# Optimization experiments

Measured on AMD Instinct MI355X. Metric: run time of the kernel, lower is better.

## Reference

```python
import jax, jax.numpy as jnp
import numpy as np

B, T, HID, MC, L, NCLS = 256, 128, 64, 30, 2, 100


def _flow(x, t, fW0, fb0, fW1, fb1, fW2, fb2, ftw):
    # Continuous affine coupling flow (stribor). x: [..., S, HID], t: [..., S, 1]
    hid = x.shape[-1]
    base = (jnp.arange(hid) < hid // 2).astype(x.dtype)  # ordered_0 mask
    for l in range(fW0.shape[0]):
        m = base if l % 2 == 0 else 1.0 - base
        z = x * m
        a = jnp.tanh(jnp.concatenate([z, t], -1) @ fW0[l] + fb0[l])
        a = jnp.tanh(a @ fW1[l] + fb1[l])
        ss = a @ fW2[l] + fb2[l]                      # [..., 2*hid]
        scale, shift = jnp.split(ss, 2, -1)
        t_scale, t_shift = jnp.split(jnp.tanh(t * ftw[l]), 2, -1)  # TimeTanh
        x = z + (1.0 - m) * (x * jnp.exp(scale * t_scale) + shift * t_shift)
    return x


def setup_inputs() -> dict:
    key = jax.random.key(0)
    ks = jax.random.split(key, 12)
    n = lambda k, s, sc=0.1: jax.random.normal(k, s, dtype=jnp.float32) * sc
    return {
        "times": jax.random.uniform(ks[0], (B, T, 1), dtype=jnp.float32),
        "marks": jax.random.randint(ks[1], (B, T, 1), 0, NCLS),
        "mask": jnp.ones((B, T, 1), jnp.float32),
        "u": jax.random.uniform(ks[2], (T, MC, 1), dtype=jnp.float32),
        "emb": n(ks[3], (NCLS, HID), 1.0),
        "fW0": n(ks[4], (L, HID + 1, HID)),
        "fb0": jnp.zeros((L, HID), jnp.float32),
        "fW1": n(ks[5], (L, HID, HID)),
        "fb1": jnp.zeros((L, HID), jnp.float32),
        "fW2": n(ks[6], (L, HID, 2 * HID)),
        "fb2": jnp.zeros((L, 2 * HID), jnp.float32),
        "ftw": n(ks[7], (L, 2 * HID), 1.0),
        "Wi": n(ks[8], (HID, 1)),
        "bi": jnp.zeros((1,), jnp.float32),
        "W_ih": n(ks[9], (4 * HID, 1 + HID)),
        "W_hh": n(ks[10], (4 * HID, HID)),
        "b_ih": jnp.zeros((4 * HID,), jnp.float32),
        "b_hh": jnp.zeros((4 * HID,), jnp.float32),
    }


def reference(times, marks, mask, u, emb, fW0, fb0, fW1, fb1, fW2, fb2, ftw,
              Wi, bi, W_ih, W_hh, b_ih, b_hh):
    Bn, Tn, _ = times.shape
    hid = emb.shape[1]
    mc = u.shape[1]
    marks_e = emb[marks[..., 0]]      # [B,T,hid]
    m1 = marks_e[:, 1]                # source uses marks[:, 1] every step (faithful)
    inten = lambda x: jax.nn.softplus(x @ Wi + bi)

    def step(carry, xs):
        h, c = carry                  # h,c: [B,hid]
        t, u_i = xs                   # t: [B,1], u_i: [mc,1]
        t3 = t[:, None, :]            # [B,1,1]
        ts = u_i[None] * t3           # [B,mc,1] MC time samples in [0,t)
        xb = jnp.broadcast_to(h[:, None, :], (Bn, mc, hid))
        path = _flow(xb, ts, fW0, fb0, fW1, fb1, fW2, fb2, ftw)   # [B,mc,hid]
        integral = inten(path).mean(1, keepdims=True) * t3        # [B,1,1]
        h2 = _flow(h[:, None, :], t3, fW0, fb0, fW1, fb1, fW2, fb2, ftw)  # [B,1,hid]
        lam = inten(h2)                                           # [B,1,1]
        gates = jnp.concatenate([t, m1], -1) @ W_ih.T + b_ih + h2[:, 0] @ W_hh.T + b_hh
        ig, fg, gg, og = jnp.split(gates, 4, -1)
        c_n = jax.nn.sigmoid(fg) * c + jax.nn.sigmoid(ig) * jnp.tanh(gg)
        h_n = jax.nn.sigmoid(og) * jnp.tanh(c_n)
        nll = -jnp.log(lam[:, 0]) + integral[:, 0]                # [B,1]
        return (h_n, c_n), (h2[:, 0], nll)

    h0 = jnp.zeros((Bn, hid), times.dtype)
    (_, _), (hidden, nll) = jax.lax.scan(step, (h0, h0), (jnp.swapaxes(times, 0, 1), u))
    hidden = jnp.swapaxes(hidden, 0, 1)                           # [B,T,hid]
    loss = (jnp.swapaxes(nll, 0, 1)[:, :, :] * mask[..., 0][..., None]).sum() / mask.sum()
    return loss, hidden
```

## Files before the change

### kernel.cpp

```cpp
#include <hip/hip_runtime.h>
#include <hip/hip_bf16.h>
#include <math.h>

#define Bn   256
#define Tn   128
#define HID  64
#define MCn  30

typedef __attribute__((ext_vector_type(8))) short bf16x8;
typedef __attribute__((ext_vector_type(4))) float f32x4;

__device__ __forceinline__ float rcp_(float x) { return __builtin_amdgcn_rcpf(x); }
__device__ __forceinline__ float tanhf_(float x) {
    float e = __expf(-2.0f * x);
    return __builtin_fmaf(2.0f, rcp_(1.0f + e), -1.0f);
}
__device__ __forceinline__ float sigmoidf_(float x) {
    return rcp_(1.0f + __expf(-x));
}
__device__ __forceinline__ float softplusf_(float z) {
    float e = __expf(-fabsf(z));
    return fmaxf(z, 0.0f) + __logf(1.0f + e);
}
__device__ __forceinline__ unsigned short f2b(float f) {
    union { float f; unsigned u; } v; v.f = f;
    unsigned r = v.u + 0x7FFF + ((v.u >> 16) & 1);
    return (unsigned short)(r >> 16);
}
__device__ __forceinline__ unsigned pk2(float a, float b) {
    union { __hip_bfloat162 h2; unsigned u; } cv;
    cv.h2 = __float22bfloat162_rn(make_float2(a, b));
    return cv.u;
}

extern "C" __global__ __launch_bounds__(256)
void prep_kernel(const int* __restrict__ marks, const float* __restrict__ mask,
                 const float* __restrict__ emb, const float* __restrict__ fW0,
                 const float* __restrict__ fW1, const float* __restrict__ fW2,
                 const float* __restrict__ fb0, const float* __restrict__ fb1,
                 const float* __restrict__ fb2, const float* __restrict__ ftw,
                 const float* __restrict__ Wi, const float* __restrict__ W_ih,
                 const float* __restrict__ W_hh,
                 const float* __restrict__ b_ih, const float* __restrict__ b_hh,
                 float* __restrict__ gc, float* __restrict__ invd,
                 float* __restrict__ parv, unsigned short* __restrict__ parwb,
                 float* __restrict__ seqw1T, float* __restrict__ seqw2T,
                 float* __restrict__ whh260)
{
    __shared__ float red[4];
    const int blk = blockIdx.x, tid = threadIdx.x;
    if (blk < Bn) {
        const int mark = marks[blk * Tn + 1];
        const float* er = emb + mark * HID;
        const float* wr = W_ih + tid * 65 + 1;
        float acc = b_ih[tid] + b_hh[tid];
        #pragma unroll
        for (int k = 0; k < HID; k++) acc += er[k] * wr[k];
        gc[blk * 256 + tid] = acc;
    } else if (blk == Bn) {
        float s = 0.f;
        for (int i = tid; i < Bn * Tn; i += 256) s += mask[i];
        #pragma unroll
        for (int off = 32; off >= 1; off >>= 1) s += __shfl_xor(s, off, 64);
        if ((tid & 63) == 0) red[tid >> 6] = s;
        __syncthreads();
        if (tid == 0) invd[0] = 1.0f / (red[0] + red[1] + red[2] + red[3]);
    } else if (blk == Bn + 1) {
        if (tid < 128) {
            int l = tid >> 6, m = tid & 63;
            parv[tid]       = fb0[tid];
            parv[128 + tid] = fW0[(l * 65 + 64) * 64 + m];
            parv[256 + tid] = fb1[tid];
            int act = 32 * (1 - l);
            parv[384 + tid] = fb2[l * 128 + act + (m & 31) + 64 * (m >> 5)];
        }
        if (tid < 64) {
            int l = tid >> 5, i2 = tid & 31, act = 32 * (1 - l);
            parv[512 + tid] = ftw[l * 128 + act + i2];
            parv[576 + tid] = ftw[l * 128 + 64 + act + i2];
            parv[640 + tid] = Wi[tid];
            parv[704 + tid] = 0.f;
        }
    } else if (blk == Bn + 2) {
        for (int i = tid; i < 5120; i += 256) {
            int k = i % 40, m = (i / 40) & 63, l = i / 2560;
            float v = (k < 32) ? fW0[(l * 65 + 32 * l + k) * 64 + m] : 0.f;
            parwb[i] = f2b(v);
        }
    } else if (blk == Bn + 3) {
        for (int i = tid; i < 9216; i += 256) {
            int k = i % 72, m = (i / 72) & 63, l = i / 4608;
            float v = (k < 64) ? fW1[(l * 64 + k) * 64 + m] : 0.f;
            parwb[5120 + i] = f2b(v);
        }
    } else if (blk == Bn + 4) {
        for (int i = tid; i < 9216; i += 256) {
            int k = i % 72, m = (i / 72) & 63, l = i / 4608;
            int act = 32 * (1 - l);
            float v = (k < 64) ? fW2[(l * 64 + k) * 128 + act + (m & 31) + 64 * (m >> 5)] : 0.f;
            parwb[14336 + i] = f2b(v);
        }
    } else if (blk == Bn + 5) {
        for (int i = tid; i < 8704; i += 256) {
            int k = i % 68, j = (i / 68) & 63, l = i / 4352;
            seqw1T[i] = (k < 64) ? fW1[(l * 64 + k) * 64 + j] : 0.f;
        }
    } else if (blk == Bn + 6) {
        for (int i = tid; i < 8704; i += 256) {
            int k = i % 68, j = (i / 68) & 63, l = i / 4352;
            int act = 32 * (1 - l);
            seqw2T[i] = (k < 64) ?
                fW2[(l * 64 + k) * 128 + act + (j & 31) + 64 * (j >> 5)] : 0.f;
        }
    } else {
        for (int i = tid; i < 16640; i += 256) {
            int j = i / 260, rem = i % 260, k = rem >> 2, r = rem & 3;
            whh260[i] = (k < 64) ? W_hh[(r * 64 + j) * 64 + k] : 0.f;
        }
    }
}

extern "C" __global__ __launch_bounds__(64, 1)
void seq_kernel(const float* __restrict__ times, const float* __restrict__ mask,
                const float* __restrict__ fW0, const float* __restrict__ fb0,
                const float* __restrict__ fb1, const float* __restrict__ fb2,
                const float* __restrict__ ftw, const float* __restrict__ Wi,
                const float* __restrict__ bi, const float* __restrict__ W_ih,
                const float* __restrict__ gc, const float* __restrict__ seqw1T,
                const float* __restrict__ invd,
                float* __restrict__ h_carry, float* __restrict__ out)
{
    const int j = threadIdx.x;
    const int b = blockIdx.x;

    extern __shared__ float smem[];
    float* w1l  = smem;
    float* w2l  = smem + 8704;
    float* whhl = smem + 17408;
    float* tl   = smem + 34048;
    float* ml   = smem + 34176;
    float* xl   = smem + 34304;
    float* al   = smem + 34368;
    float* ssl  = smem + 34432;

    {
        const float4* s = (const float4*)seqw1T;
        float4* d = (float4*)smem;
        for (int i = j; i < 8512; i += 64) d[i] = s[i];
    }
    tl[j] = times[b * Tn + j];       tl[j + 64] = times[b * Tn + 64 + j];
    ml[j] = mask[b * Tn + j];        ml[j + 64] = mask[b * Tn + 64 + j];

    float w0c[2][32], w0tc[2], b0c[2], b1c[2], b2c[2], ftsc[2], ftsh[2];
    #pragma unroll
    for (int l = 0; l < 2; l++) {
        #pragma unroll
        for (int kk = 0; kk < 32; kk++)
            w0c[l][kk] = fW0[(l * 65 + 32 * l + kk) * 64 + j];
        w0tc[l] = fW0[(l * 65 + 64) * 64 + j];
        b0c[l]  = fb0[l * 64 + j];
        b1c[l]  = fb1[l * 64 + j];
        const int act = 32 * (1 - l);
        b2c[l]  = fb2[l * 128 + act + (j & 31) + 64 * (j >> 5)];
        ftsc[l] = ftw[l * 128 + j];
        ftsh[l] = ftw[l * 128 + 64 + j];
    }
    const float wij = Wi[j];
    const float bi0 = bi[0];
    float wih0[4], gcr[4];
    #pragma unroll
    for (int r = 0; r < 4; r++) {
        wih0[r] = W_ih[(r * 64 + j) * 65];
        gcr[r]  = gc[b * 256 + r * 64 + j];
    }
    const float idn = invd[0];

    float h = 0.f, c = 0.f, nllacc = 0.f;
    for (int t = 0; t < Tn; t++) {
        const float tb = tl[t];
        float tscv[2], tshv[2];
        #pragma unroll
        for (int l = 0; l < 2; l++) {
            tscv[l] = tanhf_(tb * ftsc[l]);
            tshv[l] = tanhf_(tb * ftsh[l]);
        }
        h_carry[(b * Tn + t) * 64 + j] = h;
        float x = h;
        xl[j] = x;
        #pragma unroll
        for (int l = 0; l < 2; l++) {
            const int kb  = 32 * l;
            const int act = 32 * (1 - l);
            float p0 = b0c[l] + tb * w0tc[l], p1 = 0.f, p2 = 0.f, p3 = 0.f;
            {
                const float4* xv4 = (const float4*)(xl + kb);
                #pragma unroll
                for (int k4 = 0; k4 < 8; k4++) {
                    float4 xv = xv4[k4];
                    p0 += xv.x * w0c[l][4 * k4 + 0];
                    p1 += xv.y * w0c[l][4 * k4 + 1];
                    p2 += xv.z * w0c[l][4 * k4 + 2];
                    p3 += xv.w * w0c[l][4 * k4 + 3];
                }
            }
            al[j] = tanhf_((p0 + p1) + (p2 + p3));
            p0 = b1c[l]; p1 = p2 = p3 = 0.f;
            {
                const float4* av4 = (const float4*)al;
                const float*  wp  = w1l + (l * 64 + j) * 68;
                #pragma unroll
                for (int k4 = 0; k4 < 16; k4++) {
                    float4 av = av4[k4];
                    float4 wv = *(const float4*)(wp + 4 * k4);
                    p0 += av.x * wv.x;
                    p1 += av.y * wv.y;
                    p2 += av.z * wv.z;
                    p3 += av.w * wv.w;
                }
            }
            al[j] = tanhf_((p0 + p1) + (p2 + p3));
            p0 = b2c[l]; p1 = p2 = p3 = 0.f;
            {
                const float4* av4 = (const float4*)al;
                const float*  wp  = w2l + (l * 64 + j) * 68;
                #pragma unroll
                for (int k4 = 0; k4 < 16; k4++) {
                    float4 av = av4[k4];
                    float4 wv = *(const float4*)(wp + 4 * k4);
                    p0 += av.x * wv.x;
                    p1 += av.y * wv.y;
                    p2 += av.z * wv.z;
                    p3 += av.w * wv.w;
                }
            }
            ssl[j] = (p0 + p1) + (p2 + p3);
            const int idx = (j - act) & 31;
            const float scl = ssl[idx];
            const float shf = ssl[idx + 32];
            const float xa  = x * __expf(scl * tscv[l]) + shf * tshv[l];
            const bool active = (l == 0) ? (j >= 32) : (j < 32);
            x = active ? xa : x;
            xl[j] = x;
        }
        out[1 + (b * Tn + t) * 64 + j] = x;
        float v = x * wij;
        #pragma unroll
        for (int off = 32; off >= 1; off >>= 1) v += __shfl_xor(v, off, 64);
        nllacc += -__logf(softplusf_(v + bi0)) * ml[t];
        float g0 = gcr[0] + tb * wih0[0];
        float g1 = gcr[1] + tb * wih0[1];
        float g2 = gcr[2] + tb * wih0[2];
        float g3 = gcr[3] + tb * wih0[3];
        {
            const float*  wr_base = whhl + j * 260;
            const float4* hv4 = (const float4*)xl;
            #pragma unroll
            for (int k4 = 0; k4 < 16; k4++) {
                float4 hv = hv4[k4];
                const float* wr = wr_base + 16 * k4;
                float4 wa = *(const float4*)(wr);
                float4 wb = *(const float4*)(wr + 4);
                float4 wc = *(const float4*)(wr + 8);
                float4 wd = *(const float4*)(wr + 12);
                g0 += hv.x * wa.x; g1 += hv.x * wa.y; g2 += hv.x * wa.z; g3 += hv.x * wa.w;
                g0 += hv.y * wb.x; g1 += hv.y * wb.y; g2 += hv.y * wb.z; g3 += hv.y * wb.w;
                g0 += hv.z * wc.x; g1 += hv.z * wc.y; g2 += hv.z * wc.z; g3 += hv.z * wc.w;
                g0 += hv.w * wd.x; g1 += hv.w * wd.y; g2 += hv.w * wd.z; g3 += hv.w * wd.w;
            }
        }
        c = sigmoidf_(g1) * c + sigmoidf_(g0) * tanhf_(g2);
        h = sigmoidf_(g3) * tanhf_(c);
    }
    if (j == 0) atomicAdd(out, nllacc * idn);
}

extern "C" __global__ __launch_bounds__(256, 2)
void par_kernel(const float* __restrict__ times, const float* __restrict__ mask,
                const float* __restrict__ u, const float* __restrict__ bi,
                const float* __restrict__ invd, const float* __restrict__ parv,
                const unsigned short* __restrict__ parwb,
                const float* __restrict__ h_carry, float* __restrict__ pp)
{
    __shared__ __align__(16) unsigned short sact[128 * 72];
    __shared__ __align__(16) unsigned short sxk1[128 * 40];
    __shared__ __align__(16) unsigned short sx0b[4 * 40];
    __shared__ float pr[4];

    const int tid = threadIdx.x, lane = tid & 63, w = tid >> 6;
    const int quad = lane >> 4, l15 = lane & 15;

    const int q = blockIdx.x * 4 + w;
    const int t = q >> 8, b = q & 255;
    const float tb = times[b * Tn + t];
    const float* hrow = h_carry + (b * Tn + t) * 64;
    if (lane < 32) sx0b[w * 40 + lane] = f2b(hrow[lane]);

    float tsv[2], sclf[2];
    {
        const float base = tb * (1.0f / 30.0f) * invd[0] * mask[b * Tn + t];
        #pragma unroll
        for (int nt = 0; nt < 2; nt++) {
            int mc = nt * 16 + l15;
            bool val = (mc < 30);
            tsv[nt]  = val ? u[t * MCn + mc] * tb : 0.f;
            sclf[nt] = val ? base : 0.f;
        }
    }
    f32x4 xr[2][4];
    #pragma unroll
    for (int mt = 0; mt < 4; mt++) {
        f32x4 v = *(const f32x4*)(hrow + mt * 16 + quad * 4);
        xr[0][mt] = v; xr[1][mt] = v;
    }
    const int srow = w * 32;

    #pragma unroll
    for (int l = 0; l < 2; l++) {
        const unsigned short* wA1 = parwb + l * 2560;
        const unsigned short* wA2 = parwb + 5120 + l * 4608;
        const unsigned short* wA3 = parwb + 14336 + l * 4608;
        f32x4 c1[4][2];
        if (l == 0) {
            bf16x8 bb = *(const bf16x8*)(sx0b + w * 40 + quad * 8);
            #pragma unroll
            for (int mt = 0; mt < 4; mt++) {
                bf16x8 af = *(const bf16x8*)(wA1 + (mt * 16 + l15) * 40 + quad * 8);
                f32x4 z = {0.f, 0.f, 0.f, 0.f};
                c1[mt][0] = __builtin_amdgcn_mfma_f32_16x16x32_bf16(af, bb, z, 0, 0, 0);
                c1[mt][1] = c1[mt][0];
            }
        } else {
            bf16x8 bf[2];
            #pragma unroll
            for (int nt = 0; nt < 2; nt++)
                bf[nt] = *(const bf16x8*)(sxk1 + (srow + nt * 16 + l15) * 40 + quad * 8);
            #pragma unroll
            for (int mt = 0; mt < 4; mt++) {
                bf16x8 af = *(const bf16x8*)(wA1 + (mt * 16 + l15) * 40 + quad * 8);
                #pragma unroll
                for (int nt = 0; nt < 2; nt++) {
                    f32x4 z = {0.f, 0.f, 0.f, 0.f};
                    c1[mt][nt] = __builtin_amdgcn_mfma_f32_16x16x32_bf16(af, bf[nt], z, 0, 0, 0);
                }
            }
        }
        #pragma unroll
        for (int mt = 0; mt < 4; mt++) {
            f32x4 b0r = *(const f32x4*)(parv + 0   + l * 64 + mt * 16 + quad * 4);
            f32x4 w0r = *(const f32x4*)(parv + 128 + l * 64 + mt * 16 + quad * 4);
            #pragma unroll
            for (int nt = 0; nt < 2; nt++) {
                float v0 = tanhf_(c1[mt][nt][0] + b0r[0] + tsv[nt] * w0r[0]);
                float v1 = tanhf_(c1[mt][nt][1] + b0r[1] + tsv[nt] * w0r[1]);
                float v2 = tanhf_(c1[mt][nt][2] + b0r[2] + tsv[nt] * w0r[2]);
                float v3 = tanhf_(c1[mt][nt][3] + b0r[3] + tsv[nt] * w0r[3]);
                uint2 pk; pk.x = pk2(v0, v1); pk.y = pk2(v2, v3);
                *(uint2*)(sact + (srow + nt * 16 + l15) * 72 + mt * 16 + quad * 4) = pk;
            }
        }
        f32x4 cc[4][2];
        #pragma unroll
        for (int mt = 0; mt < 4; mt++)
            #pragma unroll
            for (int nt = 0; nt < 2; nt++) cc[mt][nt] = (f32x4){0.f, 0.f, 0.f, 0.f};
        #pragma unroll
        for (int kt = 0; kt < 2; kt++) {
            bf16x8 bf[2];
            #pragma unroll
            for (int nt = 0; nt < 2; nt++)
                bf[nt] = *(const bf16x8*)(sact + (srow + nt * 16 + l15) * 72 + kt * 32 + quad * 8);
            #pragma unroll
            for (int mt = 0; mt < 4; mt++) {
                bf16x8 af = *(const bf16x8*)(wA2 + (mt * 16 + l15) * 72 + kt * 32 + quad * 8);
                #pragma unroll
                for (int nt = 0; nt < 2; nt++)
                    cc[mt][nt] = __builtin_amdgcn_mfma_f32_16x16x32_bf16(af, bf[nt], cc[mt][nt], 0, 0, 0);
            }
        }
        #pragma unroll
        for (int mt = 0; mt < 4; mt++) {
            f32x4 b1r = *(const f32x4*)(parv + 256 + l * 64 + mt * 16 + quad * 4);
            #pragma unroll
            for (int nt = 0; nt < 2; nt++) {
                float v0 = tanhf_(cc[mt][nt][0] + b1r[0]);
                float v1 = tanhf_(cc[mt][nt][1] + b1r[1]);
                float v2 = tanhf_(cc[mt][nt][2] + b1r[2]);
                float v3 = tanhf_(cc[mt][nt][3] + b1r[3]);
                uint2 pk; pk.x = pk2(v0, v1); pk.y = pk2(v2, v3);
                *(uint2*)(sact + (srow + nt * 16 + l15) * 72 + mt * 16 + quad * 4) = pk;
            }
        }
        f32x4 ssf[4][2];
        #pragma unroll
        for (int mt = 0; mt < 4; mt++)
            #pragma unroll
            for (int nt = 0; nt < 2; nt++) ssf[mt][nt] = (f32x4){0.f, 0.f, 0.f, 0.f};
        #pragma unroll
        for (int kt = 0; kt < 2; kt++) {
            bf16x8 bf[2];
            #pragma unroll
            for (int nt = 0; nt < 2; nt++)
                bf[nt] = *(const bf16x8*)(sact + (srow + nt * 16 + l15) * 72 + kt * 32 + quad * 8);
            #pragma unroll
            for (int mt = 0; mt < 4; mt++) {
                bf16x8 af = *(const bf16x8*)(wA3 + (mt * 16 + l15) * 72 + kt * 32 + quad * 8);
                #pragma unroll
                for (int nt = 0; nt < 2; nt++)
                    ssf[mt][nt] = __builtin_amdgcn_mfma_f32_16x16x32_bf16(af, bf[nt], ssf[mt][nt], 0, 0, 0);
            }
        }
        #pragma unroll
        for (int mt2 = 0; mt2 < 2; mt2++) {
            f32x4 b2s = *(const f32x4*)(parv + 384 + l * 64 +      mt2 * 16 + quad * 4);
            f32x4 b2h = *(const f32x4*)(parv + 384 + l * 64 + 32 + mt2 * 16 + quad * 4);
            f32x4 fa  = *(const f32x4*)(parv + 512 + l * 32 + mt2 * 16 + quad * 4);
            f32x4 fb  = *(const f32x4*)(parv + 576 + l * 32 + mt2 * 16 + quad * 4);
            const int xm = (l == 0) ? (mt2 + 2) : mt2;
            #pragma unroll
            for (int nt = 0; nt < 2; nt++) {
                #pragma unroll
                for (int r = 0; r < 4; r++) {
                    float sc  = ssf[mt2][nt][r] + b2s[r];
                    float sh  = ssf[mt2 + 2][nt][r] + b2h[r];
                    float tsc = tanhf_(tsv[nt] * fa[r]);
                    float tsh = tanhf_(tsv[nt] * fb[r]);
                    float xv  = xr[nt][xm][r];
                    xr[nt][xm][r] = xv * __expf(sc * tsc) + sh * tsh;
                }
                if (l == 0) {
                    uint2 pk;
                    pk.x = pk2(xr[nt][xm][0], xr[nt][xm][1]);
                    pk.y = pk2(xr[nt][xm][2], xr[nt][xm][3]);
                    *(uint2*)(sxk1 + (srow + nt * 16 + l15) * 40 + mt2 * 16 + quad * 4) = pk;
                }
            }
        }
    }
    float contrib = 0.f;
    const float bi0 = bi[0];
    #pragma unroll
    for (int nt = 0; nt < 2; nt++) {
        float d0 = 0.f, d1 = 0.f;
        #pragma unroll
        for (int mt = 0; mt < 4; mt++) {
            f32x4 wi4 = *(const f32x4*)(parv + 640 + mt * 16 + quad * 4);
            d0 += xr[nt][mt][0] * wi4[0] + xr[nt][mt][2] * wi4[2];
            d1 += xr[nt][mt][1] * wi4[1] + xr[nt][mt][3] * wi4[3];
        }
        float d = d0 + d1;
        d += __shfl_xor(d, 16, 64);
        d += __shfl_xor(d, 32, 64);
        contrib += softplusf_(d + bi0) * sclf[nt];
    }
    if (quad != 0) contrib = 0.f;
    #pragma unroll
    for (int off = 1; off <= 8; off <<= 1) contrib += __shfl_xor(contrib, off, 64);
    if (l15 == 0 && quad == 0) pr[w] = contrib;
    __syncthreads();
    if (tid == 0) pp[blockIdx.x] = pr[0] + pr[1] + pr[2] + pr[3];
}

extern "C" __global__ __launch_bounds__(256)
void fin_kernel(const float* __restrict__ pp, float* __restrict__ out)
{
    __shared__ float r4[4];
    const int tid = threadIdx.x;
    float s = 0.f;
    for (int i = tid; i < (Bn * Tn) / 4; i += 256) s += pp[i];
    #pragma unroll
    for (int off = 32; off >= 1; off >>= 1) s += __shfl_xor(s, off, 64);
    if ((tid & 63) == 0) r4[tid >> 6] = s;
    __syncthreads();
    if (tid == 0) atomicAdd(out, r4[0] + r4[1] + r4[2] + r4[3]);
}

extern "C" void kernel_launch(void* const* d_in, const int* in_sizes, int n_in,
                              void* d_out, int out_size, void* d_ws, size_t ws_size,
                              hipStream_t stream)
{
    const float* times = (const float*)d_in[0];
    const int*   marks = (const int*)  d_in[1];
    const float* mask  = (const float*)d_in[2];
    const float* u     = (const float*)d_in[3];
    const float* emb   = (const float*)d_in[4];
    const float* fW0   = (const float*)d_in[5];
    const float* fb0   = (const float*)d_in[6];
    const float* fW1   = (const float*)d_in[7];
    const float* fb1   = (const float*)d_in[8];
    const float* fW2   = (const float*)d_in[9];
    const float* fb2   = (const float*)d_in[10];
    const float* ftw   = (const float*)d_in[11];
    const float* Wi    = (const float*)d_in[12];
    const float* bi    = (const float*)d_in[13];
    const float* W_ih  = (const float*)d_in[14];
    const float* W_hh  = (const float*)d_in[15];
    const float* b_ih  = (const float*)d_in[16];
    const float* b_hh  = (const float*)d_in[17];
    float* out = (float*)d_out;

    float* wsp     = (float*)d_ws;
    float* h_carry = wsp;
    float* gc      = h_carry + 2097152;
    float* invd    = gc + 65536;
    float* seqw1T  = invd + 4;
    float* seqw2T  = seqw1T + 8704;
    float* whh260  = seqw2T + 8704;
    float* parv    = whh260 + 16640;
    unsigned short* parwb = (unsigned short*)(parv + 768);
    float* pp      = (float*)(parwb + 23552);

    hipMemsetAsync(d_out, 0, sizeof(float), stream);

    const int SEQ_SMEM = 34496 * 4;
    hipFuncSetAttribute((const void*)seq_kernel,
                        hipFuncAttributeMaxDynamicSharedMemorySize, SEQ_SMEM);

    prep_kernel<<<Bn + 8, 256, 0, stream>>>(marks, mask, emb, fW0, fW1, fW2,
                                            fb0, fb1, fb2, ftw, Wi, W_ih, W_hh,
                                            b_ih, b_hh, gc, invd, parv, parwb,
                                            seqw1T, seqw2T, whh260);
    seq_kernel<<<Bn, 64, SEQ_SMEM, stream>>>(times, mask, fW0, fb0, fb1, fb2,
                                             ftw, Wi, bi, W_ih, gc, seqw1T,
                                             invd, h_carry, out);
    par_kernel<<<(Bn * Tn) / 4, 256, 0, stream>>>(
        times, mask, u, bi, invd, parv, parwb, h_carry, pp);
    fin_kernel<<<1, 256, 0, stream>>>(pp, out);
}
```

Baseline: 690.1 us.

## Process two batch sequences per wavefront in the sequential LSTM-flow kernel

Each seq_kernel block now handles two batch rows (b and b+128) interleaved in one 64-lane wave, halving the grid to 128 blocks. Weight loads from shared memory are reused across both sequences, and the two independent dependency chains give instruction-level parallelism to hide latency. In exchange there are fewer blocks than CUs (256 on MI355X class), more registers per thread and a slightly larger LDS footprint, which could lengthen each block's serial time.

```diff
diff --git a/kernel.cpp b/kernel.cpp
--- a/kernel.cpp
+++ b/kernel.cpp
@@ -130,26 +130,34 @@
                 const float* __restrict__ invd,
                 float* __restrict__ h_carry, float* __restrict__ out)
 {
-    const int j = threadIdx.x;
-    const int b = blockIdx.x;
+    const int j  = threadIdx.x;
+    const int bA = blockIdx.x;
+    const int bB = blockIdx.x + 128;
 
     extern __shared__ float smem[];
     float* w1l  = smem;
     float* w2l  = smem + 8704;
     float* whhl = smem + 17408;
-    float* tl   = smem + 34048;
-    float* ml   = smem + 34176;
-    float* xl   = smem + 34304;
-    float* al   = smem + 34368;
-    float* ssl  = smem + 34432;
+    float* tlA  = smem + 34048;
+    float* tlB  = smem + 34176;
+    float* mlA  = smem + 34304;
+    float* mlB  = smem + 34432;
+    float* xlA  = smem + 34560;
+    float* xlB  = smem + 34624;
+    float* alA  = smem + 34688;
+    float* alB  = smem + 34752;
+    float* sslA = smem + 34816;
+    float* sslB = smem + 34880;
 
     {
         const float4* s = (const float4*)seqw1T;
         float4* d = (float4*)smem;
         for (int i = j; i < 8512; i += 64) d[i] = s[i];
     }
-    tl[j] = times[b * Tn + j];       tl[j + 64] = times[b * Tn + 64 + j];
-    ml[j] = mask[b * Tn + j];        ml[j + 64] = mask[b * Tn + 64 + j];
+    tlA[j] = times[bA * Tn + j];   tlA[j + 64] = times[bA * Tn + 64 + j];
+    tlB[j] = times[bB * Tn + j];   tlB[j + 64] = times[bB * Tn + 64 + j];
+    mlA[j] = mask[bA * Tn + j];    mlA[j + 64] = mask[bA * Tn + 64 + j];
+    mlB[j] = mask[bB * Tn + j];    mlB[j + 64] = mask[bB * Tn + 64 + j];
 
     float w0c[2][32], w0tc[2], b0c[2], b1c[2], b2c[2], ftsc[2], ftsh[2];
     #pragma unroll
@@ -167,111 +175,142 @@
     }
     const float wij = Wi[j];
     const float bi0 = bi[0];
-    float wih0[4], gcr[4];
+    float wih0[4], gcrA[4], gcrB[4];
     #pragma unroll
     for (int r = 0; r < 4; r++) {
         wih0[r] = W_ih[(r * 64 + j) * 65];
-        gcr[r]  = gc[b * 256 + r * 64 + j];
+        gcrA[r] = gc[bA * 256 + r * 64 + j];
+        gcrB[r] = gc[bB * 256 + r * 64 + j];
     }
     const float idn = invd[0];
 
-    float h = 0.f, c = 0.f, nllacc = 0.f;
+    float hA = 0.f, cA = 0.f, nllA = 0.f;
+    float hB = 0.f, cB = 0.f, nllB = 0.f;
     for (int t = 0; t < Tn; t++) {
-        const float tb = tl[t];
-        float tscv[2], tshv[2];
+        const float tbA = tlA[t], tbB = tlB[t];
+        float tscA[2], tshA[2], tscB[2], tshB[2];
         #pragma unroll
         for (int l = 0; l < 2; l++) {
-            tscv[l] = tanhf_(tb * ftsc[l]);
-            tshv[l] = tanhf_(tb * ftsh[l]);
-        }
-        h_carry[(b * Tn + t) * 64 + j] = h;
-        float x = h;
-        xl[j] = x;
+            tscA[l] = tanhf_(tbA * ftsc[l]);  tshA[l] = tanhf_(tbA * ftsh[l]);
+            tscB[l] = tanhf_(tbB * ftsc[l]);  tshB[l] = tanhf_(tbB * ftsh[l]);
+        }
+        h_carry[(bA * Tn + t) * 64 + j] = hA;
+        h_carry[(bB * Tn + t) * 64 + j] = hB;
+        float xA = hA, xB = hB;
+        xlA[j] = xA;  xlB[j] = xB;
         #pragma unroll
         for (int l = 0; l < 2; l++) {
             const int kb  = 32 * l;
             const int act = 32 * (1 - l);
-            float p0 = b0c[l] + tb * w0tc[l], p1 = 0.f, p2 = 0.f, p3 = 0.f;
             {
-                const float4* xv4 = (const float4*)(xl + kb);
+                float pA0 = b0c[l] + tbA * w0tc[l], pA1 = 0.f, pA2 = 0.f, pA3 = 0.f;
+                float pB0 = b0c[l] + tbB * w0tc[l], pB1 = 0.f, pB2 = 0.f, pB3 = 0.f;
+                const float4* xA4 = (const float4*)(xlA + kb);
+                const float4* xB4 = (const float4*)(xlB + kb);
                 #pragma unroll
                 for (int k4 = 0; k4 < 8; k4++) {
-                    float4 xv = xv4[k4];
-                    p0 += xv.x * w0c[l][4 * k4 + 0];
-                    p1 += xv.y * w0c[l][4 * k4 + 1];
-                    p2 += xv.z * w0c[l][4 * k4 + 2];
-                    p3 += xv.w * w0c[l][4 * k4 + 3];
+                    float4 a = xA4[k4], b = xB4[k4];
+                    pA0 += a.x * w0c[l][4 * k4 + 0];  pB0 += b.x * w0c[l][4 * k4 + 0];
+                    pA1 += a.y * w0c[l][4 * k4 + 1];  pB1 += b.y * w0c[l][4 * k4 + 1];
+                    pA2 += a.z * w0c[l][4 * k4 + 2];  pB2 += b.z * w0c[l][4 * k4 + 2];
+                    pA3 += a.w * w0c[l][4 * k4 + 3];  pB3 += b.w * w0c[l][4 * k4 + 3];
                 }
-            }
-            al[j] = tanhf_((p0 + p1) + (p2 + p3));
-            p0 = b1c[l]; p1 = p2 = p3 = 0.f;
+                alA[j] = tanhf_((pA0 + pA1) + (pA2 + pA3));
+                alB[j] = tanhf_((pB0 + pB1) + (pB2 + pB3));
+            }
             {
-                const float4* av4 = (const float4*)al;
+                float pA0 = b1c[l], pA1 = 0.f, pA2 = 0.f, pA3 = 0.f;
+                float pB0 = b1c[l], pB1 = 0.f, pB2 = 0.f, pB3 = 0.f;
+                const float4* aA4 = (const float4*)alA;
+                const float4* aB4 = (const float4*)alB;
                 const float*  wp  = w1l + (l * 64 + j) * 68;
                 #pragma unroll
                 for (int k4 = 0; k4 < 16; k4++) {
-                    float4 av = av4[k4];
                     float4 wv = *(const float4*)(wp + 4 * k4);
-                    p0 += av.x * wv.x;
-                    p1 += av.y * wv.y;
-                    p2 += av.z * wv.z;
-                    p3 += av.w * wv.w;
+                    float4 a = aA4[k4], b = aB4[k4];
+                    pA0 += a.x * wv.x;  pB0 += b.x * wv.x;
+                    pA1 += a.y * wv.y;  pB1 += b.y * wv.y;
+                    pA2 += a.z * wv.z;  pB2 += b.z * wv.z;
+                    pA3 += a.w * wv.w;  pB3 += b.w * wv.w;
                 }
-            }
-            al[j] = tanhf_((p0 + p1) + (p2 + p3));
-            p0 = b2c[l]; p1 = p2 = p3 = 0.f;
+                alA[j] = tanhf_((pA0 + pA1) + (pA2 + pA3));
+                alB[j] = tanhf_((pB0 + pB1) + (pB2 + pB3));
+            }
             {
-                const float4* av4 = (const float4*)al;
+                float pA0 = b2c[l], pA1 = 0.f, pA2 = 0.f, pA3 = 0.f;
+                float pB0 = b2c[l], pB1 = 0.f, pB2 = 0.f, pB3 = 0.f;
+                const float4* aA4 = (const float4*)alA;
+                const float4* aB4 = (const float4*)alB;
                 const float*  wp  = w2l + (l * 64 + j) * 68;
                 #pragma unroll
                 for (int k4 = 0; k4 < 16; k4++) {
-                    float4 av = av4[k4];
                     float4 wv = *(const float4*)(wp + 4 * k4);
-                    p0 += av.x * wv.x;
-                    p1 += av.y * wv.y;
-                    p2 += av.z * wv.z;
-                    p3 += av.w * wv.w;
+                    float4 a = aA4[k4], b = aB4[k4];
+                    pA0 += a.x * wv.x;  pB0 += b.x * wv.x;
+                    pA1 += a.y * wv.y;  pB1 += b.y * wv.y;
+                    pA2 += a.z * wv.z;  pB2 += b.z * wv.z;
+                    pA3 += a.w * wv.w;  pB3 += b.w * wv.w;
                 }
-            }
-            ssl[j] = (p0 + p1) + (p2 + p3);
+                sslA[j] = (pA0 + pA1) + (pA2 + pA3);
+                sslB[j] = (pB0 + pB1) + (pB2 + pB3);
+            }
             const int idx = (j - act) & 31;
-            const float scl = ssl[idx];
-            const float shf = ssl[idx + 32];
-            const float xa  = x * __expf(scl * tscv[l]) + shf * tshv[l];
             const bool active = (l == 0) ? (j >= 32) : (j < 32);
-            x = active ? xa : x;
-            xl[j] = x;
-        }
-        out[1 + (b * Tn + t) * 64 + j] = x;
-        float v = x * wij;
-        #pragma unroll
-        for (int off = 32; off >= 1; off >>= 1) v += __shfl_xor(v, off, 64);
-        nllacc += -__logf(softplusf_(v + bi0)) * ml[t];
-        float g0 = gcr[0] + tb * wih0[0];
-        float g1 = gcr[1] + tb * wih0[1];
-        float g2 = gcr[2] + tb * wih0[2];
-        float g3 = gcr[3] + tb * wih0[3];
+            {
+                const float scl = sslA[idx], shf = sslA[idx + 32];
+                const float xa  = xA * __expf(scl * tscA[l]) + shf * tshA[l];
+                xA = active ? xa : xA;
+                xlA[j] = xA;
+            }
+            {
+                const float scl = sslB[idx], shf = sslB[idx + 32];
+                const float xa  = xB * __expf(scl * tscB[l]) + shf * tshB[l];
+                xB = active ? xa : xB;
+                xlB[j] = xB;
+            }
+        }
+        out[1 + (bA * Tn + t) * 64 + j] = xA;
+        out[1 + (bB * Tn + t) * 64 + j] = xB;
+        float vA = xA * wij, vB = xB * wij;
+        #pragma unroll
+        for (int off = 32; off >= 1; off >>= 1) {
+            vA += __shfl_xor(vA, off, 64);
+            vB += __shfl_xor(vB, off, 64);
+        }
+        nllA += -__logf(softplusf_(vA + bi0)) * mlA[t];
+        nllB += -__logf(softplusf_(vB + bi0)) * mlB[t];
+        float gA0 = gcrA[0] + tbA * wih0[0], gB0 = gcrB[0] + tbB * wih0[0];
+        float gA1 = gcrA[1] + tbA * wih0[1], gB1 = gcrB[1] + tbB * wih0[1];
+        float gA2 = gcrA[2] + tbA * wih0[2], gB2 = gcrB[2] + tbB * wih0[2];
+        float gA3 = gcrA[3] + tbA * wih0[3], gB3 = gcrB[3] + tbB * wih0[3];
         {
-            const float*  wr_base = whhl + j * 260;
-            const float4* hv4 = (const float4*)xl;
+            const float* wr_base = whhl + j * 260;
+            const float4* hA4 = (const float4*)xlA;
+            const float4* hB4 = (const float4*)xlB;
             #pragma unroll
             for (int k4 = 0; k4 < 16; k4++) {
-                float4 hv = hv4[k4];
+                float4 ha = hA4[k4], hb = hB4[k4];
                 const float* wr = wr_base + 16 * k4;
                 float4 wa = *(const float4*)(wr);
                 float4 wb = *(const float4*)(wr + 4);
                 float4 wc = *(const float4*)(wr + 8);
                 float4 wd = *(const float4*)(wr + 12);
-                g0 += hv.x * wa.x; g1 += hv.x * wa.y; g2 += hv.x * wa.z; g3 += hv.x * wa.w;
-                g0 += hv.y * wb.x; g1 += hv.y * wb.y; g2 += hv.y * wb.z; g3 += hv.y * wb.w;
-                g0 += hv.z * wc.x; g1 += hv.z * wc.y; g2 += hv.z * wc.z; g3 += hv.z * wc.w;
-                g0 += hv.w * wd.x; g1 += hv.w * wd.y; g2 += hv.w * wd.z; g3 += hv.w * wd.w;
-            }
-        }
-        c = sigmoidf_(g1) * c + sigmoidf_(g0) * tanhf_(g2);
-        h = sigmoidf_(g3) * tanhf_(c);
-    }
-    if (j == 0) atomicAdd(out, nllacc * idn);
+                gA0 += ha.x * wa.x; gA1 += ha.x * wa.y; gA2 += ha.x * wa.z; gA3 += ha.x * wa.w;
+                gB0 += hb.x * wa.x; gB1 += hb.x * wa.y; gB2 += hb.x * wa.z; gB3 += hb.x * wa.w;
+                gA0 += ha.y * wb.x; gA1 += ha.y * wb.y; gA2 += ha.y * wb.z; gA3 += ha.y * wb.w;
+                gB0 += hb.y * wb.x; gB1 += hb.y * wb.y; gB2 += hb.y * wb.z; gB3 += hb.y * wb.w;
+                gA0 += ha.z * wc.x; gA1 += ha.z * wc.y; gA2 += ha.z * wc.z; gA3 += ha.z * wc.w;
+                gB0 += hb.z * wc.x; gB1 += hb.z * wc.y; gB2 += hb.z * wc.z; gB3 += hb.z * wc.w;
+                gA0 += ha.w * wd.x; gA1 += ha.w * wd.y; gA2 += ha.w * wd.z; gA3 += ha.w * wd.w;
+                gB0 += hb.w * wd.x; gB1 += hb.w * wd.y; gB2 += hb.w * wd.z; gB3 += hb.w * wd.w;
+            }
+        }
+        cA = sigmoidf_(gA1) * cA + sigmoidf_(gA0) * tanhf_(gA2);
+        hA = sigmoidf_(gA3) * tanhf_(cA);
+        cB = sigmoidf_(gB1) * cB + sigmoidf_(gB0) * tanhf_(gB2);
+        hB = sigmoidf_(gB3) * tanhf_(cB);
+    }
+    if (j == 0) atomicAdd(out, (nllA + nllB) * idn);
 }
 
 extern "C" __global__ __launch_bounds__(256, 2)
@@ -511,7 +550,7 @@
 
     hipMemsetAsync(d_out, 0, sizeof(float), stream);
 
-    const int SEQ_SMEM = 34496 * 4;
+    const int SEQ_SMEM = 34944 * 4;
     hipFuncSetAttribute((const void*)seq_kernel,
                         hipFuncAttributeMaxDynamicSharedMemorySize, SEQ_SMEM);
 
@@ -519,9 +558,9 @@
                                             fb0, fb1, fb2, ftw, Wi, W_ih, W_hh,
                                             b_ih, b_hh, gc, invd, parv, parwb,
                                             seqw1T, seqw2T, whh260);
-    seq_kernel<<<Bn, 64, SEQ_SMEM, stream>>>(times, mask, fW0, fb0, fb1, fb2,
-                                             ftw, Wi, bi, W_ih, gc, seqw1T,
-                                             invd, h_carry, out);
+    seq_kernel<<<Bn / 2, 64, SEQ_SMEM, stream>>>(times, mask, fW0, fb0, fb1, fb2,
+                                                 ftw, Wi, bi, W_ih, gc, seqw1T,
+                                                 invd, h_carry, out);
     par_kernel<<<(Bn * Tn) / 4, 256, 0, stream>>>(
         times, mask, u, bi, invd, parv, parwb, h_carry, pp);
     fin_kernel<<<1, 256, 0, stream>>>(pp, out);
```

New measurement: 920.9 us. 33.4% more time.
